# Optimization experiments

Hardware: AMD Instinct MI355X
Metric: run time of the kernel (lower is better)

The kernel has to match this reference:

```python
import jax, jax.numpy as jnp
import numpy as np

EPS = 1e-6
LN_EPS = 1e-5   # torch nn.LayerNorm default eps
BN_EPS = 1e-5   # torch nn.BatchNorm1d default eps
NUM_HEADS = 8
NEG_SLOPE = 0.0  # leaky=0 in TransformerBlock


def vn_linear(x, W, b, eps=1e-6):
    # x: [B, Cin, 3, N], W: [Cin, Cout], b: [Cout, 3]
    out = jnp.einsum('bidn,io->bodn', x, W)
    u = eps * b / jnp.linalg.norm(b, axis=1, keepdims=True)  # [Cout,3]
    return out + u[None, :, :, None]


def vn_layer_norm(x, gamma, beta):
    # x: [B, C, 3, N]; LayerNorm over channel dim of the vector norms
    norm = jnp.linalg.norm(x, axis=2) + EPS            # [B, C, N]
    t = jnp.swapaxes(norm, 1, 2)                       # [B, N, C]
    mu = t.mean(axis=-1, keepdims=True)
    var = ((t - mu) ** 2).mean(axis=-1, keepdims=True)
    ln = (t - mu) / jnp.sqrt(var + LN_EPS) * gamma + beta
    norm_ln = jnp.swapaxes(ln, 1, 2)                   # [B, C, N]
    return x / norm[:, :, None, :] * norm_ln[:, :, None, :]


def vn_batch_norm(x, gamma, beta):
    # training-mode BatchNorm1d over channel dim of the vector norms
    norm = jnp.linalg.norm(x, axis=2) + EPS            # [B, C, N]
    mu = norm.mean(axis=(0, 2), keepdims=True)         # [1, C, 1]
    var = ((norm - mu) ** 2).mean(axis=(0, 2), keepdims=True)
    bn = (norm - mu) / jnp.sqrt(var + BN_EPS) * gamma[None, :, None] + beta[None, :, None]
    return x / norm[:, :, None, :] * bn[:, :, None, :]


def vn_leaky_relu(x, W, negative_slope=NEG_SLOPE):
    d = jnp.einsum('bidn,io->bodn', x, W)              # learned direction
    dot = (x * d).sum(axis=2, keepdims=True)           # [B, C, 1, N]
    d_norm_sq = (d * d).sum(axis=2, keepdims=True)
    proj = x - dot / (d_norm_sq + EPS) * d
    pos = jnp.where(dot >= 0, x, proj)
    return negative_slope * x + (1.0 - negative_slope) * pos


def attention(Q, K, Z, Wq, bq, Wk, bk, Wz, bz, Wo, bo, num_heads=NUM_HEADS):
    B, C, _, M = Q.shape
    N = K.shape[-1]
    Ch = C // num_heads
    q = vn_linear(Q, Wq, bq).reshape(B, num_heads, Ch, 3, M)
    k = vn_linear(K, Wk, bk).reshape(B, num_heads, Ch, 3, N)
    z = vn_linear(Z, Wz, bz).reshape(B, num_heads, Ch, 3, N)
    # Frobenius inner product: merge (Ch,3) -> F
    qf = q.reshape(B, num_heads, Ch * 3, M)
    kf = k.reshape(B, num_heads, Ch * 3, N)
    const = 1.0 / np.sqrt(3 * Ch)
    scores = const * jnp.einsum('bhfm,bhfn->bhmn', qf, kf)
    A = jax.nn.softmax(scores, axis=-1)
    out = jnp.einsum('bhcdn,bhmn->bhcdm', z, A).reshape(B, C, 3, M)
    return vn_linear(out, Wo, bo)


def forward(x, Wq, bq, Wk, bk, Wz, bz, Wo, bo, ln1_g, ln1_b,
            Wm1, bm1, bn_g, bn_b, Wr, Wm2, bm2, ln2_g, ln2_b):
    queries = x
    y = attention(queries, x, x, Wq, bq, Wk, bk, Wz, bz, Wo, bo)
    y = vn_layer_norm(y, ln1_g, ln1_b)
    y = y + queries
    identity = y
    h = vn_linear(y, Wm1, bm1)
    h = vn_batch_norm(h, bn_g, bn_b)
    h = vn_leaky_relu(h, Wr)
    h = vn_linear(h, Wm2, bm2)
    h = vn_layer_norm(h, ln2_g, ln2_b)
    return h + identity


def setup_inputs() -> dict:
    key = jax.random.key(0)
    ks = list(jax.random.split(key, 16))
    B, C, N = 8, 256, 1024
    bound = 1.0 / np.sqrt(C)

    def lin(k, fin, fout):
        k1, k2 = jax.random.split(k)
        W = jax.random.uniform(k1, (fin, fout), minval=-bound, maxval=bound, dtype=jnp.float32)
        b = jax.random.uniform(k2, (fout, 3), minval=-bound, maxval=bound, dtype=jnp.float32)
        return W, b

    x = jax.random.normal(ks[0], (B, C, 3, N), dtype=jnp.float32)
    Wq, bq = lin(ks[1], C, C)
    Wk, bk = lin(ks[2], C, C)
    Wz, bz = lin(ks[3], C, C)
    Wo, bo = lin(ks[4], C, C)
    Wm1, bm1 = lin(ks[5], C, C)
    Wm2, bm2 = lin(ks[6], C, C)
    Wr = jax.random.uniform(ks[7], (C, C), minval=-bound, maxval=bound, dtype=jnp.float32)
    ones = jnp.ones((C,), jnp.float32)
    zeros = jnp.zeros((C,), jnp.float32)
    return dict(x=x, Wq=Wq, bq=bq, Wk=Wk, bk=bk, Wz=Wz, bz=bz, Wo=Wo, bo=bo,
                ln1_g=ones, ln1_b=zeros, Wm1=Wm1, bm1=bm1, bn_g=ones, bn_b=zeros,
                Wr=Wr, Wm2=Wm2, bm2=bm2, ln2_g=ones, ln2_b=zeros)


def reference(x, Wq, bq, Wk, bk, Wz, bz, Wo, bo, ln1_g, ln1_b,
              Wm1, bm1, bn_g, bn_b, Wr, Wm2, bm2, ln2_g, ln2_b):
    return forward(x, Wq, bq, Wk, bk, Wz, bz, Wo, bo, ln1_g, ln1_b,
                   Wm1, bm1, bn_g, bn_b, Wr, Wm2, bm2, ln2_g, ln2_b)
```

## Files before the change

kernel.cpp:

```cpp
#include <hip/hip_runtime.h>
#include <math.h>

typedef __attribute__((ext_vector_type(8))) short bf16x8;
typedef __attribute__((ext_vector_type(4))) float f32x4;
typedef unsigned short u16;
typedef __attribute__((ext_vector_type(4))) unsigned short u16x4;
typedef __attribute__((ext_vector_type(8))) unsigned short u16x8;
typedef __attribute__((ext_vector_type(4))) unsigned int u32x4;

#define VN_EPS 1e-6f
#define LN_EPS 1e-5f
#define BN_EPS 1e-5f
#define ISQ 0.10206207261596575f

__device__ __forceinline__ u16 f2bf(float f) {
    unsigned u = __builtin_bit_cast(unsigned, f);
    return (u16)((u + 0x7FFFu + ((u >> 16) & 1u)) >> 16);
}
__device__ __forceinline__ float bf2f(u16 h) {
    unsigned u = ((unsigned)h) << 16;
    return __builtin_bit_cast(float, u);
}

__global__ __launch_bounds__(256) void k_u(
    const float* __restrict__ b0, const float* __restrict__ b1,
    const float* __restrict__ b2, const float* __restrict__ b3,
    const float* __restrict__ b4, const float* __restrict__ b5,
    float* __restrict__ uall)
{
    const float* bs[6] = {b0, b1, b2, b3, b4, b5};
    const float* bp = bs[blockIdx.x];
    const int co = threadIdx.x;
    const float v0 = bp[co*3+0], v1 = bp[co*3+1], v2 = bp[co*3+2];
    const float inv = rsqrtf(v0*v0 + v1*v1 + v2*v2);
    float* u = uall + blockIdx.x*768 + co*3;
    u[0] = VN_EPS*v0*inv; u[1] = VN_EPS*v1*inv; u[2] = VN_EPS*v2*inv;
}

__global__ __launch_bounds__(256) void k_wtrans(
    const float* __restrict__ w0, const float* __restrict__ w1,
    const float* __restrict__ w2, const float* __restrict__ w3,
    const float* __restrict__ w4, const float* __restrict__ w5,
    const float* __restrict__ w6, u16* __restrict__ wth, u16* __restrict__ wtl)
{
    const int wi = blockIdx.z;
    const float* W = (wi==0)?w0:(wi==1)?w1:(wi==2)?w2:(wi==3)?w3:(wi==4)?w4:(wi==5)?w5:w6;
    u16* WtH = wth + (long)wi*65536;
    u16* WtL = wtl + (long)wi*65536;
    const int i0 = blockIdx.y*64, o0 = blockIdx.x*64;
    __shared__ float st[64][67];
    const int t = threadIdx.x, q = t >> 6, lane = t & 63;
    for (int j = 0; j < 16; ++j) {
        const int i = q*16 + j;
        st[i][lane] = W[(i0 + i)*256 + o0 + lane];
    }
    __syncthreads();
    for (int j = 0; j < 16; ++j) {
        const int o = q*16 + j;
        const float v = st[lane][o];
        const u16 hi = f2bf(v);
        WtH[(o0 + o)*256 + i0 + lane] = hi;
        WtL[(o0 + o)*256 + i0 + lane] = f2bf(v - bf2f(hi));
    }
}

template<int MODE>
__global__ __launch_bounds__(256) void k_cgemm(
    const float* __restrict__ X, const u16* __restrict__ WtH, const u16* __restrict__ WtL,
    const float* __restrict__ U,
    float* __restrict__ OutF, u16* __restrict__ OutH, u16* __restrict__ OutL)
{
    __shared__ u16 sh[32768];
    const int tid = threadIdx.x;
    const int b = blockIdx.z / 3, d = blockIdx.z % 3;
    const int n0 = blockIdx.x * 64;
    const int co0 = blockIdx.y * 64;

    {
        const int tn = (tid & 15) * 4;
        const int ti = (tid >> 4) * 4;
        #pragma unroll
        for (int it = 0; it < 4; ++it) {
            const int i_l = it*64 + ti;
            const long rb = (((long)(b*256 + i_l))*3 + d)*1024 + n0 + tn;
            const float4 r0 = *(const float4*)&X[rb];
            const float4 r1 = *(const float4*)&X[rb + 3072];
            const float4 r2 = *(const float4*)&X[rb + 6144];
            const float4 r3 = *(const float4*)&X[rb + 9216];
            const float vals[4][4] = {
                {r0.x, r1.x, r2.x, r3.x},
                {r0.y, r1.y, r2.y, r3.y},
                {r0.z, r1.z, r2.z, r3.z},
                {r0.w, r1.w, r2.w, r3.w}};
            #pragma unroll
            for (int j = 0; j < 4; ++j) {
                const int n = tn + j;
                u16x4 hv, lv;
                #pragma unroll
                for (int e = 0; e < 4; ++e) {
                    const float v = vals[j][e];
                    const u16 hi = f2bf(v);
                    hv[e] = hi;
                    lv[e] = f2bf(v - bf2f(hi));
                }
                const int slot = i_l >> 3;
                const int idx = n*256 + ((((slot ^ (n & 7)) << 3)) | (i_l & 4));
                *(u16x4*)&sh[idx] = hv;
                *(u16x4*)&sh[16384 + idx] = lv;
            }
        }
    }
    __syncthreads();

    const int w = tid >> 6, l = tid & 63;
    const int lr = l & 15, lg = l >> 4;

    f32x4 zero = {0.f, 0.f, 0.f, 0.f};
    f32x4 acc[4] = {zero, zero, zero, zero};

    const long arow = (long)(co0 + w*16 + lr)*256 + lg*8;
    #pragma unroll
    for (int s = 0; s < 8; ++s) {
        const bf16x8 ah = *(const bf16x8*)(WtH + arow + s*32);
        const bf16x8 al = *(const bf16x8*)(WtL + arow + s*32);
        #pragma unroll
        for (int ni = 0; ni < 4; ++ni) {
            const int row = ni*16 + lr;
            const int slot = s*4 + lg;
            const int idx = row*256 + ((slot ^ (row & 7)) << 3);
            const bf16x8 bh_ = *(const bf16x8*)&sh[idx];
            const bf16x8 bl_ = *(const bf16x8*)&sh[16384 + idx];
            acc[ni] = __builtin_amdgcn_mfma_f32_16x16x32_bf16(ah, bh_, acc[ni], 0, 0, 0);
            acc[ni] = __builtin_amdgcn_mfma_f32_16x16x32_bf16(ah, bl_, acc[ni], 0, 0, 0);
            acc[ni] = __builtin_amdgcn_mfma_f32_16x16x32_bf16(al, bh_, acc[ni], 0, 0, 0);
        }
    }

    if constexpr (MODE == 0) {
        #pragma unroll
        for (int ni = 0; ni < 4; ++ni)
            #pragma unroll
            for (int r = 0; r < 4; ++r) {
                const int co = co0 + w*16 + lg*4 + r;
                const int nn = n0 + ni*16 + lr;
                float v = acc[ni][r];
                if (U) v += U[co*3 + d];
                OutF[(((long)(b*256 + co))*3 + d)*1024 + nn] = v;
            }
    } else if constexpr (MODE == 1) {
        #pragma unroll
        for (int ni = 0; ni < 4; ++ni)
            #pragma unroll
            for (int r = 0; r < 4; ++r) {
                const int co = co0 + w*16 + lg*4 + r;
                const int nn = n0 + ni*16 + lr;
                float v = acc[ni][r] + U[co*3 + d];
                const long idx = (((long)(b*256 + co))*3 + d)*1024 + nn;
                const u16 hi = f2bf(v);
                OutH[idx] = hi;
                OutL[idx] = f2bf(v - bf2f(hi));
            }
    } else {
        __syncthreads();
        u16* olh = sh;
        u16* oll = sh + 8448;
        #pragma unroll
        for (int ni = 0; ni < 4; ++ni)
            #pragma unroll
            for (int r = 0; r < 4; ++r) {
                const int co_l = w*16 + lg*4 + r;
                float v = acc[ni][r] + U[(co0 + co_l)*3 + d];
                const u16 hi = f2bf(v);
                olh[co_l*66 + ni*16 + lr] = hi;
                oll[co_l*66 + ni*16 + lr] = f2bf(v - bf2f(hi));
            }
        __syncthreads();
        const int n_l = tid & 63, grp = tid >> 6;
        const int h = (co0 >> 5) + (grp >> 1);
        const long base = ((long)(b*8 + h)*1024 + n0 + n_l)*96 + d*32 + (grp & 1)*16;
        u16x8 v0h, v1h, v0l, v1l;
        #pragma unroll
        for (int p = 0; p < 8; ++p) {
            v0h[p] = olh[(grp*16 + p)*66 + n_l];
            v1h[p] = olh[(grp*16 + 8 + p)*66 + n_l];
            v0l[p] = oll[(grp*16 + p)*66 + n_l];
            v1l[p] = oll[(grp*16 + 8 + p)*66 + n_l];
        }
        *(u16x8*)&OutH[base]     = v0h;
        *(u16x8*)&OutH[base + 8] = v1h;
        *(u16x8*)&OutL[base]     = v0l;
        *(u16x8*)&OutL[base + 8] = v1l;
    }
}

__global__ __launch_bounds__(256) void k_attn(
    const u16* __restrict__ Qh, const u16* __restrict__ Ql,
    const u16* __restrict__ Kh, const u16* __restrict__ Kl,
    const u16* __restrict__ Zh, const u16* __restrict__ Zl,
    float* __restrict__ Ao)
{
    const int i = blockIdx.x;
    const int xcd = i & 7;
    const int j = i >> 3;
    const int bh = xcd*8 + (j >> 4);
    const int mt = j & 15;
    const int b = bh >> 3, h = bh & 7;
    const int tid = threadIdx.x;
    const int w = tid >> 6, l = tid & 63, lr = l & 15, lg = l >> 4;
    const int m0 = mt*64 + w*16;

    __shared__ u16 khi[64*104], klo[64*104];
    __shared__ u16 zhi[96*72],  zlo[96*72];

    f32x4 zero = {0.f, 0.f, 0.f, 0.f};

    const long qbase = ((long)bh*1024 + m0 + lr)*96 + lg*8;
    bf16x8 qhf[3], qlf[3];
    #pragma unroll
    for (int s = 0; s < 3; ++s) {
        qhf[s] = *(const bf16x8*)(Qh + qbase + s*32);
        qlf[s] = *(const bf16x8*)(Ql + qbase + s*32);
    }

    f32x4 acc2[6];
    #pragma unroll
    for (int f = 0; f < 6; ++f) acc2[f] = zero;
    float run_m = -1e30f, run_l = 0.f;

    const long zrow = (long)(b*768 + h*96);
    const int sAl = lr + ((lg & 1) << 5);
    const int sBl = sAl + 16;
    const bool hiT = (lg & 2) != 0;

    for (int c = 0; c < 16; ++c) {
        const int n0 = c*64;
        __syncthreads();
        {
            const long kgb = ((long)bh*1024 + n0)*96;
            #pragma unroll
            for (int it = 0; it < 3; ++it) {
                const int id = it*256 + tid;
                const int row = id / 12, off = (id % 12)*8;
                *(u16x8*)&khi[row*104 + off] = *(const u16x8*)(Kh + kgb + id*8);
                *(u16x8*)&klo[row*104 + off] = *(const u16x8*)(Kl + kgb + id*8);
            }
            #pragma unroll
            for (int it = 0; it < 3; ++it) {
                const int id = it*256 + tid;
                const int f = id >> 3, off = (id & 7)*8;
                const long zg = (zrow + f)*1024 + n0 + off;
                *(u16x8*)&zhi[f*72 + off] = *(const u16x8*)(Zh + zg);
                *(u16x8*)&zlo[f*72 + off] = *(const u16x8*)(Zl + zg);
            }
        }
        __syncthreads();

        f32x4 sc[4];
        #pragma unroll
        for (int t = 0; t < 4; ++t) {
            const int krow = (t*16 + lr)*104 + lg*8;
            f32x4 a = zero;
            #pragma unroll
            for (int s = 0; s < 3; ++s) {
                const bf16x8 khf = *(const bf16x8*)&khi[krow + s*32];
                const bf16x8 klf = *(const bf16x8*)&klo[krow + s*32];
                a = __builtin_amdgcn_mfma_f32_16x16x32_bf16(khf, qhf[s], a, 0, 0, 0);
                a = __builtin_amdgcn_mfma_f32_16x16x32_bf16(khf, qlf[s], a, 0, 0, 0);
                a = __builtin_amdgcn_mfma_f32_16x16x32_bf16(klf, qhf[s], a, 0, 0, 0);
            }
            sc[t] = a;
        }

        float tmax = -1e30f;
        #pragma unroll
        for (int t = 0; t < 4; ++t)
            #pragma unroll
            for (int r = 0; r < 4; ++r)
                tmax = fmaxf(tmax, sc[t][r]);
        tmax = fmaxf(tmax, __shfl_xor(tmax, 16));
        tmax = fmaxf(tmax, __shfl_xor(tmax, 32));
        const float m_new = fmaxf(run_m, tmax);
        const float fr = __expf((run_m - m_new)*ISQ);
        float sm = 0.f;
        #pragma unroll
        for (int t = 0; t < 4; ++t)
            #pragma unroll
            for (int r = 0; r < 4; ++r) {
                const float p = __expf((sc[t][r] - m_new)*ISQ);
                sc[t][r] = p;
                sm += p;
            }
        sm += __shfl_xor(sm, 16);
        sm += __shfl_xor(sm, 32);
        run_l = run_l * fr + sm;
        run_m = m_new;
        #pragma unroll
        for (int r = 0; r < 4; ++r) {
            const float fm = __shfl(fr, lg*4 + r);
            #pragma unroll
            for (int ff = 0; ff < 6; ++ff) acc2[ff][r] *= fm;
        }

        #pragma unroll
        for (int kb = 0; kb < 2; ++kb) {
            const f32x4 pA = sc[2*kb], pB = sc[2*kb + 1];
            const u16 a0 = f2bf(pA[0]), a1 = f2bf(pA[1]), a2 = f2bf(pA[2]), a3 = f2bf(pA[3]);
            const u16 b0 = f2bf(pB[0]), b1 = f2bf(pB[1]), b2 = f2bf(pB[2]), b3 = f2bf(pB[3]);
            const unsigned ah01 = (unsigned)a0 | ((unsigned)a1 << 16);
            const unsigned ah23 = (unsigned)a2 | ((unsigned)a3 << 16);
            const unsigned bh01 = (unsigned)b0 | ((unsigned)b1 << 16);
            const unsigned bh23 = (unsigned)b2 | ((unsigned)b3 << 16);
            const unsigned al01 = (unsigned)f2bf(pA[0]-bf2f(a0)) | ((unsigned)f2bf(pA[1]-bf2f(a1)) << 16);
            const unsigned al23 = (unsigned)f2bf(pA[2]-bf2f(a2)) | ((unsigned)f2bf(pA[3]-bf2f(a3)) << 16);
            const unsigned bl01 = (unsigned)f2bf(pB[0]-bf2f(b0)) | ((unsigned)f2bf(pB[1]-bf2f(b1)) << 16);
            const unsigned bl23 = (unsigned)f2bf(pB[2]-bf2f(b2)) | ((unsigned)f2bf(pB[3]-bf2f(b3)) << 16);

            const unsigned hA01 = (unsigned)__shfl((int)ah01, sAl), hB01 = (unsigned)__shfl((int)bh01, sAl);
            const unsigned hA23 = (unsigned)__shfl((int)ah23, sAl), hB23 = (unsigned)__shfl((int)bh23, sAl);
            const unsigned hA45 = (unsigned)__shfl((int)ah01, sBl), hB45 = (unsigned)__shfl((int)bh01, sBl);
            const unsigned hA67 = (unsigned)__shfl((int)ah23, sBl), hB67 = (unsigned)__shfl((int)bh23, sBl);
            const unsigned lA01 = (unsigned)__shfl((int)al01, sAl), lB01 = (unsigned)__shfl((int)bl01, sAl);
            const unsigned lA23 = (unsigned)__shfl((int)al23, sAl), lB23 = (unsigned)__shfl((int)bl23, sAl);
            const unsigned lA45 = (unsigned)__shfl((int)al01, sBl), lB45 = (unsigned)__shfl((int)bl01, sBl);
            const unsigned lA67 = (unsigned)__shfl((int)al23, sBl), lB67 = (unsigned)__shfl((int)bl23, sBl);

            const u32x4 th = { hiT ? hB01 : hA01, hiT ? hB23 : hA23,
                               hiT ? hB45 : hA45, hiT ? hB67 : hA67 };
            const u32x4 tl = { hiT ? lB01 : lA01, hiT ? lB23 : lA23,
                               hiT ? lB45 : lA45, hiT ? lB67 : lA67 };
            const bf16x8 pah = __builtin_bit_cast(bf16x8, th);
            const bf16x8 pal = __builtin_bit_cast(bf16x8, tl);

            #pragma unroll
            for (int ff = 0; ff < 6; ++ff) {
                const int zoff = (ff*16 + lr)*72 + kb*32 + lg*8;
                const bf16x8 zh8 = *(const bf16x8*)&zhi[zoff];
                const bf16x8 zl8 = *(const bf16x8*)&zlo[zoff];
                acc2[ff] = __builtin_amdgcn_mfma_f32_16x16x32_bf16(pah, zh8, acc2[ff], 0, 0, 0);
                acc2[ff] = __builtin_amdgcn_mfma_f32_16x16x32_bf16(pah, zl8, acc2[ff], 0, 0, 0);
                acc2[ff] = __builtin_amdgcn_mfma_f32_16x16x32_bf16(pal, zh8, acc2[ff], 0, 0, 0);
            }
        }
    }

    const float lrec = 1.0f / run_l;
    #pragma unroll
    for (int r = 0; r < 4; ++r) {
        const float iv = __shfl(lrec, lg*4 + r);
        #pragma unroll
        for (int ff = 0; ff < 6; ++ff) acc2[ff][r] *= iv;
    }
    #pragma unroll
    for (int ff = 0; ff < 6; ++ff) {
        #pragma unroll
        for (int r = 0; r < 4; ++r)
            Ao[(zrow + ff*16 + lr)*1024 + m0 + lg*4 + r] = acc2[ff][r];
    }
}

__global__ __launch_bounds__(256) void k_vnln(
    const float* __restrict__ X, const float* __restrict__ Res,
    const float* __restrict__ g, const float* __restrict__ be,
    float* __restrict__ Out)
{
    const int b  = blockIdx.x >> 5;
    const int n  = ((blockIdx.x & 31) << 5) + threadIdx.x;
    const int ty = threadIdx.y;
    const long bbase = (long)b * (256*3*1024);
    float sum = 0.0f, sq = 0.0f;
    for (int ci = 0; ci < 32; ++ci) {
        const int c = (ty << 5) + ci;
        const long base = bbase + (long)c*3072 + n;
        const float x0 = X[base], x1 = X[base+1024], x2 = X[base+2048];
        const float nr = sqrtf(x0*x0 + x1*x1 + x2*x2) + VN_EPS;
        sum += nr; sq += nr*nr;
    }
    __shared__ float s_sum[8][32], s_sq[8][32];
    s_sum[ty][threadIdx.x] = sum; s_sq[ty][threadIdx.x] = sq;
    __syncthreads();
    __shared__ float s_mu[32], s_rs[32];
    if (ty == 0) {
        float S = 0.0f, Q = 0.0f;
        #pragma unroll
        for (int w = 0; w < 8; ++w) { S += s_sum[w][threadIdx.x]; Q += s_sq[w][threadIdx.x]; }
        const float mu = S / 256.0f;
        s_mu[threadIdx.x] = mu;
        s_rs[threadIdx.x] = rsqrtf(Q / 256.0f - mu*mu + LN_EPS);
    }
    __syncthreads();
    const float mu = s_mu[threadIdx.x], rstd = s_rs[threadIdx.x];
    for (int ci = 0; ci < 32; ++ci) {
        const int c = (ty << 5) + ci;
        const long base = bbase + (long)c*3072 + n;
        const float x0 = X[base], x1 = X[base+1024], x2 = X[base+2048];
        const float nr = sqrtf(x0*x0 + x1*x1 + x2*x2) + VN_EPS;
        const float ln = (nr - mu) * rstd * g[c] + be[c];
        const float s  = ln / nr;
        float o0 = x0*s, o1 = x1*s, o2 = x2*s;
        if (Res) { o0 += Res[base]; o1 += Res[base+1024]; o2 += Res[base+2048]; }
        Out[base] = o0; Out[base+1024] = o1; Out[base+2048] = o2;
    }
}

__global__ __launch_bounds__(256) void k_bnstats(
    const float* __restrict__ X, float* __restrict__ bnst)
{
    const int c = blockIdx.x;
    const int t = threadIdx.x;
    float sum = 0.0f, sq = 0.0f;
    for (int b = 0; b < 8; ++b) {
        const long rowbase = ((long)(b*256 + c)) * 3072;
        for (int n0 = 0; n0 < 1024; n0 += 256) {
            const int n = n0 + t;
            const float x0 = X[rowbase + n], x1 = X[rowbase + 1024 + n], x2 = X[rowbase + 2048 + n];
            const float nr = sqrtf(x0*x0 + x1*x1 + x2*x2) + VN_EPS;
            sum += nr; sq += nr*nr;
        }
    }
    #pragma unroll
    for (int off = 32; off > 0; off >>= 1) {
        sum += __shfl_xor(sum, off);
        sq  += __shfl_xor(sq,  off);
    }
    __shared__ float rs[4], rq[4];
    if ((t & 63) == 0) { rs[t >> 6] = sum; rq[t >> 6] = sq; }
    __syncthreads();
    if (t == 0) {
        const float S = rs[0]+rs[1]+rs[2]+rs[3];
        const float Q = rq[0]+rq[1]+rq[2]+rq[3];
        const float mu = S / 8192.0f;
        bnst[c] = mu;
        bnst[256 + c] = rsqrtf(Q / 8192.0f - mu*mu + BN_EPS);
    }
}

__global__ __launch_bounds__(256) void k_bnapply(
    float* __restrict__ X, const float* __restrict__ bnst,
    const float* __restrict__ g, const float* __restrict__ be)
{
    const long i = (long)blockIdx.x * 256 + threadIdx.x;
    const int  n  = (int)(i & 1023);
    const long bc = i >> 10;
    const int  c  = (int)(bc & 255);
    const long base = bc * 3072 + n;
    const float x0 = X[base], x1 = X[base+1024], x2 = X[base+2048];
    const float nr = sqrtf(x0*x0 + x1*x1 + x2*x2) + VN_EPS;
    const float bn = (nr - bnst[c]) * bnst[256 + c] * g[c] + be[c];
    const float s  = bn / nr;
    X[base]      = x0*s;
    X[base+1024] = x1*s;
    X[base+2048] = x2*s;
}

__global__ __launch_bounds__(256) void k_leaky(
    float* __restrict__ X, const float* __restrict__ Dd)
{
    const long i = (long)blockIdx.x * 256 + threadIdx.x;
    const long base = (i >> 10) * 3072 + (i & 1023);
    const float x0 = X[base], x1 = X[base+1024], x2 = X[base+2048];
    const float d0 = Dd[base], d1 = Dd[base+1024], d2 = Dd[base+2048];
    const float dot = x0*d0 + x1*d1 + x2*d2;
    if (dot < 0.0f) {
        const float f = dot / (d0*d0 + d1*d1 + d2*d2 + VN_EPS);
        X[base]      = x0 - f*d0;
        X[base+1024] = x1 - f*d1;
        X[base+2048] = x2 - f*d2;
    }
}

extern "C" void kernel_launch(void* const* d_in, const int* in_sizes, int n_in,
                              void* d_out, int out_size, void* d_ws, size_t ws_size,
                              hipStream_t stream)
{
    const float* x    = (const float*)d_in[0];
    const float* Wq   = (const float*)d_in[1];
    const float* bq   = (const float*)d_in[2];
    const float* Wk   = (const float*)d_in[3];
    const float* bk   = (const float*)d_in[4];
    const float* Wz   = (const float*)d_in[5];
    const float* bz   = (const float*)d_in[6];
    const float* Wo   = (const float*)d_in[7];
    const float* bo   = (const float*)d_in[8];
    const float* ln1g = (const float*)d_in[9];
    const float* ln1b = (const float*)d_in[10];
    const float* Wm1  = (const float*)d_in[11];
    const float* bm1  = (const float*)d_in[12];
    const float* bng  = (const float*)d_in[13];
    const float* bnb  = (const float*)d_in[14];
    const float* Wr   = (const float*)d_in[15];
    const float* Wm2  = (const float*)d_in[16];
    const float* bm2  = (const float*)d_in[17];
    const float* ln2g = (const float*)d_in[18];
    const float* ln2b = (const float*)d_in[19];
    float* out = (float*)d_out;

    char* wsb = (char*)d_ws;
    u16*   qh  = (u16*)(wsb + 0);
    u16*   ql  = (u16*)(wsb + 12582912);
    u16*   kh  = (u16*)(wsb + 25165824);
    u16*   kl  = (u16*)(wsb + 37748736);
    u16*   zh  = (u16*)(wsb + 50331648);
    u16*   zl  = (u16*)(wsb + 62914560);
    u16*   wth = (u16*)(wsb + 109051904);
    u16*   wtl = (u16*)(wsb + 109969408);
    float* uall= (float*)(wsb + 110886912);
    float* bnst= (float*)(wsb + 110905344);
    float* ao  = out;
    float* y0f = (float*)(wsb + 0);
    float* y   = (float*)(wsb + 25165824);
    float* h   = (float*)(wsb + 50331648);
    float* dv  = (float*)(wsb + 75497472);
    float* h2  = (float*)(wsb + 0);

    const dim3 GC(16, 4, 24);

    k_u<<<6, 256, 0, stream>>>(bq, bk, bz, bo, bm1, bm2, uall);
    k_wtrans<<<dim3(4,4,7), 256, 0, stream>>>(Wq, Wk, Wz, Wo, Wm1, Wr, Wm2, wth, wtl);

    k_cgemm<2><<<GC, 256, 0, stream>>>(x, wth + 0*65536, wtl + 0*65536, uall + 0*768, nullptr, qh, ql);
    k_cgemm<2><<<GC, 256, 0, stream>>>(x, wth + 1*65536, wtl + 1*65536, uall + 1*768, nullptr, kh, kl);
    k_cgemm<1><<<GC, 256, 0, stream>>>(x, wth + 2*65536, wtl + 2*65536, uall + 2*768, nullptr, zh, zl);

    k_attn<<<1024, 256, 0, stream>>>(qh, ql, kh, kl, zh, zl, ao);

    k_cgemm<0><<<GC, 256, 0, stream>>>(ao, wth + 3*65536, wtl + 3*65536, uall + 3*768, y0f, nullptr, nullptr);
    k_vnln<<<256, dim3(32,8), 0, stream>>>(y0f, x, ln1g, ln1b, y);

    k_cgemm<0><<<GC, 256, 0, stream>>>(y, wth + 4*65536, wtl + 4*65536, uall + 4*768, h, nullptr, nullptr);
    k_bnstats<<<256, 256, 0, stream>>>(h, bnst);
    k_bnapply<<<8192, 256, 0, stream>>>(h, bnst, bng, bnb);
    k_cgemm<0><<<GC, 256, 0, stream>>>(h, wth + 5*65536, wtl + 5*65536, (const float*)nullptr, dv, nullptr, nullptr);
    k_leaky<<<8192, 256, 0, stream>>>(h, dv);
    k_cgemm<0><<<GC, 256, 0, stream>>>(h, wth + 6*65536, wtl + 6*65536, uall + 5*768, h2, nullptr, nullptr);
    k_vnln<<<256, dim3(32,8), 0, stream>>>(h2, y, ln2g, ln2b, out);
}
```

Baseline: 484.7 us.

## Share one LDS buffer for K and Z in attention, fold score scale into Q

The attention kernel now reuses a single pair of shared-memory buffers for the K tile and then the Z tile. Z is loaded after the softmax step, behind an extra barrier. This roughly halves LDS use per block so more blocks can fit on a CU, but Z loads can no longer overlap the score MFMAs. The 1/sqrt(3*Ch) softmax scale is folded into the Q projection epilogue through a new scale argument, removing per-element multiplies in the exp computation. Output stores are vectorized to float4.

```diff
diff --git a/kernel.cpp b/kernel.cpp
--- a/kernel.cpp
+++ b/kernel.cpp
@@ -68,7 +68,7 @@
 __global__ __launch_bounds__(256) void k_cgemm(
     const float* __restrict__ X, const u16* __restrict__ WtH, const u16* __restrict__ WtL,
     const float* __restrict__ U,
-    float* __restrict__ OutF, u16* __restrict__ OutH, u16* __restrict__ OutL)
+    float* __restrict__ OutF, u16* __restrict__ OutH, u16* __restrict__ OutL, float scale)
 {
     __shared__ u16 sh[32768];
     const int tid = threadIdx.x;
@@ -169,7 +169,7 @@
             #pragma unroll
             for (int r = 0; r < 4; ++r) {
                 const int co_l = w*16 + lg*4 + r;
-                float v = acc[ni][r] + U[(co0 + co_l)*3 + d];
+                float v = (acc[ni][r] + U[(co0 + co_l)*3 + d]) * scale;
                 const u16 hi = f2bf(v);
                 olh[co_l*66 + ni*16 + lr] = hi;
                 oll[co_l*66 + ni*16 + lr] = f2bf(v - bf2f(hi));
@@ -209,8 +209,7 @@
     const int w = tid >> 6, l = tid & 63, lr = l & 15, lg = l >> 4;
     const int m0 = mt*64 + w*16;
 
-    __shared__ u16 khi[64*104], klo[64*104];
-    __shared__ u16 zhi[96*72],  zlo[96*72];
+    __shared__ u16 bufh[6912], bufl[6912];
 
     f32x4 zero = {0.f, 0.f, 0.f, 0.f};
 
@@ -241,16 +240,8 @@
             for (int it = 0; it < 3; ++it) {
                 const int id = it*256 + tid;
                 const int row = id / 12, off = (id % 12)*8;
-                *(u16x8*)&khi[row*104 + off] = *(const u16x8*)(Kh + kgb + id*8);
-                *(u16x8*)&klo[row*104 + off] = *(const u16x8*)(Kl + kgb + id*8);
-            }
-            #pragma unroll
-            for (int it = 0; it < 3; ++it) {
-                const int id = it*256 + tid;
-                const int f = id >> 3, off = (id & 7)*8;
-                const long zg = (zrow + f)*1024 + n0 + off;
-                *(u16x8*)&zhi[f*72 + off] = *(const u16x8*)(Zh + zg);
-                *(u16x8*)&zlo[f*72 + off] = *(const u16x8*)(Zl + zg);
+                *(u16x8*)&bufh[row*104 + off] = *(const u16x8*)(Kh + kgb + id*8);
+                *(u16x8*)&bufl[row*104 + off] = *(const u16x8*)(Kl + kgb + id*8);
             }
         }
         __syncthreads();
@@ -262,8 +253,8 @@
             f32x4 a = zero;
             #pragma unroll
             for (int s = 0; s < 3; ++s) {
-                const bf16x8 khf = *(const bf16x8*)&khi[krow + s*32];
-                const bf16x8 klf = *(const bf16x8*)&klo[krow + s*32];
+                const bf16x8 khf = *(const bf16x8*)&bufh[krow + s*32];
+                const bf16x8 klf = *(const bf16x8*)&bufl[krow + s*32];
                 a = __builtin_amdgcn_mfma_f32_16x16x32_bf16(khf, qhf[s], a, 0, 0, 0);
                 a = __builtin_amdgcn_mfma_f32_16x16x32_bf16(khf, qlf[s], a, 0, 0, 0);
                 a = __builtin_amdgcn_mfma_f32_16x16x32_bf16(klf, qhf[s], a, 0, 0, 0);
@@ -280,13 +271,13 @@
         tmax = fmaxf(tmax, __shfl_xor(tmax, 16));
         tmax = fmaxf(tmax, __shfl_xor(tmax, 32));
         const float m_new = fmaxf(run_m, tmax);
-        const float fr = __expf((run_m - m_new)*ISQ);
+        const float fr = __expf(run_m - m_new);
         float sm = 0.f;
         #pragma unroll
         for (int t = 0; t < 4; ++t)
             #pragma unroll
             for (int r = 0; r < 4; ++r) {
-                const float p = __expf((sc[t][r] - m_new)*ISQ);
+                const float p = __expf(sc[t][r] - m_new);
                 sc[t][r] = p;
                 sm += p;
             }
@@ -300,6 +291,19 @@
             #pragma unroll
             for (int ff = 0; ff < 6; ++ff) acc2[ff][r] *= fm;
         }
+
+        __syncthreads();
+        {
+            #pragma unroll
+            for (int it = 0; it < 3; ++it) {
+                const int id = it*256 + tid;
+                const int f = id >> 3, off = (id & 7)*8;
+                const long zg = (zrow + f)*1024 + n0 + off;
+                *(u16x8*)&bufh[f*72 + off] = *(const u16x8*)(Zh + zg);
+                *(u16x8*)&bufl[f*72 + off] = *(const u16x8*)(Zl + zg);
+            }
+        }
+        __syncthreads();
 
         #pragma unroll
         for (int kb = 0; kb < 2; ++kb) {
@@ -334,8 +338,8 @@
             #pragma unroll
             for (int ff = 0; ff < 6; ++ff) {
                 const int zoff = (ff*16 + lr)*72 + kb*32 + lg*8;
-                const bf16x8 zh8 = *(const bf16x8*)&zhi[zoff];
-                const bf16x8 zl8 = *(const bf16x8*)&zlo[zoff];
+                const bf16x8 zh8 = *(const bf16x8*)&bufh[zoff];
+                const bf16x8 zl8 = *(const bf16x8*)&bufl[zoff];
                 acc2[ff] = __builtin_amdgcn_mfma_f32_16x16x32_bf16(pah, zh8, acc2[ff], 0, 0, 0);
                 acc2[ff] = __builtin_amdgcn_mfma_f32_16x16x32_bf16(pah, zl8, acc2[ff], 0, 0, 0);
                 acc2[ff] = __builtin_amdgcn_mfma_f32_16x16x32_bf16(pal, zh8, acc2[ff], 0, 0, 0);
@@ -352,9 +356,9 @@
     }
     #pragma unroll
     for (int ff = 0; ff < 6; ++ff) {
-        #pragma unroll
-        for (int r = 0; r < 4; ++r)
-            Ao[(zrow + ff*16 + lr)*1024 + m0 + lg*4 + r] = acc2[ff][r];
+        float4 o;
+        o.x = acc2[ff][0]; o.y = acc2[ff][1]; o.z = acc2[ff][2]; o.w = acc2[ff][3];
+        *(float4*)&Ao[(zrow + ff*16 + lr)*1024 + m0 + lg*4] = o;
     }
 }
 
@@ -517,20 +521,20 @@
     k_u<<<6, 256, 0, stream>>>(bq, bk, bz, bo, bm1, bm2, uall);
     k_wtrans<<<dim3(4,4,7), 256, 0, stream>>>(Wq, Wk, Wz, Wo, Wm1, Wr, Wm2, wth, wtl);
 
-    k_cgemm<2><<<GC, 256, 0, stream>>>(x, wth + 0*65536, wtl + 0*65536, uall + 0*768, nullptr, qh, ql);
-    k_cgemm<2><<<GC, 256, 0, stream>>>(x, wth + 1*65536, wtl + 1*65536, uall + 1*768, nullptr, kh, kl);
-    k_cgemm<1><<<GC, 256, 0, stream>>>(x, wth + 2*65536, wtl + 2*65536, uall + 2*768, nullptr, zh, zl);
+    k_cgemm<2><<<GC, 256, 0, stream>>>(x, wth + 0*65536, wtl + 0*65536, uall + 0*768, nullptr, qh, ql, ISQ);
+    k_cgemm<2><<<GC, 256, 0, stream>>>(x, wth + 1*65536, wtl + 1*65536, uall + 1*768, nullptr, kh, kl, 1.0f);
+    k_cgemm<1><<<GC, 256, 0, stream>>>(x, wth + 2*65536, wtl + 2*65536, uall + 2*768, nullptr, zh, zl, 1.0f);
 
     k_attn<<<1024, 256, 0, stream>>>(qh, ql, kh, kl, zh, zl, ao);
 
-    k_cgemm<0><<<GC, 256, 0, stream>>>(ao, wth + 3*65536, wtl + 3*65536, uall + 3*768, y0f, nullptr, nullptr);
+    k_cgemm<0><<<GC, 256, 0, stream>>>(ao, wth + 3*65536, wtl + 3*65536, uall + 3*768, y0f, nullptr, nullptr, 1.0f);
     k_vnln<<<256, dim3(32,8), 0, stream>>>(y0f, x, ln1g, ln1b, y);
 
-    k_cgemm<0><<<GC, 256, 0, stream>>>(y, wth + 4*65536, wtl + 4*65536, uall + 4*768, h, nullptr, nullptr);
+    k_cgemm<0><<<GC, 256, 0, stream>>>(y, wth + 4*65536, wtl + 4*65536, uall + 4*768, h, nullptr, nullptr, 1.0f);
     k_bnstats<<<256, 256, 0, stream>>>(h, bnst);
     k_bnapply<<<8192, 256, 0, stream>>>(h, bnst, bng, bnb);
-    k_cgemm<0><<<GC, 256, 0, stream>>>(h, wth + 5*65536, wtl + 5*65536, (const float*)nullptr, dv, nullptr, nullptr);
+    k_cgemm<0><<<GC, 256, 0, stream>>>(h, wth + 5*65536, wtl + 5*65536, (const float*)nullptr, dv, nullptr, nullptr, 1.0f);
     k_leaky<<<8192, 256, 0, stream>>>(h, dv);
-    k_cgemm<0><<<GC, 256, 0, stream>>>(h, wth + 6*65536, wtl + 6*65536, uall + 5*768, h2, nullptr, nullptr);
+    k_cgemm<0><<<GC, 256, 0, stream>>>(h, wth + 6*65536, wtl + 6*65536, uall + 5*768, h2, nullptr, nullptr, 1.0f);
     k_vnln<<<256, dim3(32,8), 0, stream>>>(h2, y, ln2g, ln2b, out);
 }
```

Result: faster. 474.7 us (-2.1%).
